# Optimization experiments

Hardware: AMD Instinct MI355X
Metric: run time of the kernel (lower is better)

The kernel has to match this reference:

```python
import jax, jax.numpy as jnp
import numpy as np

B, L = 8, 512
EMB, NHEAD, HD = 512, 8, 64
FFN, NL = 2048, 6
VOCAB, NRE, RING_START, PAD, MAXLEN = 45, 20, 24, 0, 512
NOUT0 = VOCAB - NRE  # 25
NEG = -jnp.inf


def _ln(x, g, b, eps=1e-5):
    m = jnp.mean(x, -1, keepdims=True)
    v = jnp.mean((x - m) ** 2, -1, keepdims=True)
    return (x - m) * jax.lax.rsqrt(v + eps) * g + b


def setup_inputs():
    key = jax.random.key(0)
    ks = jax.random.split(key, 24)
    p = lambda k, shape: jax.random.normal(k, shape, jnp.float32) * 0.02
    return {
        "sequences": jax.random.randint(ks[0], (B, L), 1, VOCAB),  # avoid PAD=0
        "count_sequences": jax.random.randint(ks[1], (B, L), 0, MAXLEN),
        "graph_mask_sequences": jax.random.bernoulli(ks[2], 0.05, (B, L, VOCAB)),
        "valence_mask_sequences": jax.random.bernoulli(ks[3], 0.05, (B, L, VOCAB)),
        "linear_loc_squares": jax.random.randint(ks[4], (B, L, L), 0, MAXLEN + 1),
        "up_loc_squares": jax.random.randint(ks[5], (B, L, L), 0, MAXLEN + 1),
        "down_loc_squares": jax.random.randint(ks[6], (B, L, L), 0, MAXLEN + 1),
        "tok_emb": p(ks[7], (VOCAB, EMB)),
        "cnt_emb": p(ks[8], (MAXLEN, EMB)),
        "lin_loc_emb": p(ks[9], (MAXLEN + 1, NHEAD)),
        "up_loc_emb": p(ks[10], (MAXLEN + 1, NHEAD)),
        "down_loc_emb": p(ks[11], (MAXLEN + 1, NHEAD)),
        "in_proj_w": p(ks[12], (NL, 3 * EMB, EMB)),
        "in_proj_b": jnp.zeros((NL, 3 * EMB), jnp.float32),
        "out_w": p(ks[13], (NL, EMB, EMB)),
        "out_b": jnp.zeros((NL, EMB), jnp.float32),
        "ln1_g": jnp.ones((NL, EMB), jnp.float32),
        "ln1_b": jnp.zeros((NL, EMB), jnp.float32),
        "ln2_g": jnp.ones((NL, EMB), jnp.float32),
        "ln2_b": jnp.zeros((NL, EMB), jnp.float32),
        "ffn_w1": p(ks[14], (NL, FFN, EMB)),
        "ffn_b1": jnp.zeros((NL, FFN), jnp.float32),
        "ffn_w2": p(ks[15], (NL, EMB, FFN)),
        "ffn_b2": jnp.zeros((NL, EMB), jnp.float32),
        "fin_g": jnp.ones((EMB,), jnp.float32),
        "fin_b": jnp.zeros((EMB,), jnp.float32),
        "gen_w": p(ks[16], (NOUT0, EMB)),
        "gen_b": jnp.zeros((NOUT0,), jnp.float32),
        "ring_w0": p(ks[17], (EMB, EMB)),
        "ring_b0": jnp.zeros((EMB,), jnp.float32),
        "ring_w1": p(ks[18], (EMB, EMB)),
        "ring_b1": jnp.zeros((EMB,), jnp.float32),
    }


def _forward(tok_emb, cnt_emb, lin_loc_emb, up_loc_emb, down_loc_emb,
             in_proj_w, in_proj_b, out_w, out_b, ln1_g, ln1_b, ln2_g, ln2_b,
             ffn_w1, ffn_b1, ffn_w2, ffn_b2, fin_g, fin_b, gen_w, gen_b,
             ring_w0, ring_b0, ring_w1, ring_b1,
             sequences, count_sequences, graph_mask_sequences,
             valence_mask_sequences, linear_loc_squares, up_loc_squares,
             down_loc_squares):
    scale_e = jnp.sqrt(jnp.float32(EMB))
    x = tok_emb[sequences] * scale_e + cnt_emb[count_sequences] * scale_e  # (B,L,E)

    # per-head additive attention bias from three (B,L,L) index lookups
    bias = lin_loc_emb[linear_loc_squares] + up_loc_emb[up_loc_squares] + down_loc_emb[down_loc_squares]  # (B,L,L,H)
    bias = jnp.transpose(bias, (0, 3, 1, 2))  # (B,H,Lq,Lk)
    causal = jnp.tril(jnp.ones((L, L), bool))
    attn_bias = jnp.where(causal[None, None], bias, NEG)
    pad = sequences == PAD  # key padding
    attn_bias = jnp.where(pad[:, None, None, :], NEG, attn_bias)

    inv_sqrt_hd = 1.0 / jnp.sqrt(jnp.float32(HD))
    for i in range(NL):  # post-norm TransformerEncoderLayer, gelu
        qkv = jnp.einsum('ble,fe->blf', x, in_proj_w[i]) + in_proj_b[i]
        q, k, v = jnp.split(qkv, 3, axis=-1)
        q = q.reshape(B, L, NHEAD, HD)
        k = k.reshape(B, L, NHEAD, HD)
        v = v.reshape(B, L, NHEAD, HD)
        scores = jnp.einsum('bqhd,bkhd->bhqk', q, k) * inv_sqrt_hd + attn_bias
        a = jax.nn.softmax(scores, axis=-1)
        ctx = jnp.einsum('bhqk,bkhd->bqhd', a, v).reshape(B, L, EMB)
        attn_out = jnp.einsum('ble,fe->blf', ctx, out_w[i]) + out_b[i]
        x = _ln(x + attn_out, ln1_g[i], ln1_b[i])
        h = jax.nn.gelu(jnp.einsum('ble,fe->blf', x, ffn_w1[i]) + ffn_b1[i], approximate=False)
        ff = jnp.einsum('blf,ef->ble', h, ffn_w2[i]) + ffn_b2[i]
        x = _ln(x + ff, ln2_g[i], ln2_b[i])
    x = _ln(x, fin_g, fin_b)

    logits0 = jnp.einsum('ble,oe->blo', x, gen_w) + gen_b  # (B,L,NOUT0)

    # EdgeLogitLayer: scatter ring-start projections into NRE slots
    out0 = jnp.einsum('ble,he->blh', x, ring_w0) + ring_b0
    out1_ = jnp.einsum('ble,he->blh', x, ring_w1) + ring_b1
    ring_start = sequences == RING_START
    idx = jnp.where(ring_start, jnp.cumsum(ring_start.astype(jnp.int32), axis=1), 0)  # (B,L)
    bidx = jnp.arange(B)[:, None]
    slots = jnp.zeros((B, NRE + 1, EMB), x.dtype).at[bidx, idx].set(out1_, mode='drop')
    ring_tab = slots[:, 1:]  # drop slot 0 (non-ring-start writes)
    logits1 = jnp.einsum('ble,bre->blr', out0, ring_tab) * (EMB ** -0.5)

    logits = jnp.concatenate([logits0, logits1], axis=2)  # (B,L,VOCAB)
    logits = jnp.where(graph_mask_sequences, NEG, logits)
    logits = jnp.where(valence_mask_sequences, NEG, logits)
    return logits


def reference(sequences, count_sequences, graph_mask_sequences, valence_mask_sequences,
              linear_loc_squares, up_loc_squares, down_loc_squares,
              tok_emb, cnt_emb, lin_loc_emb, up_loc_emb, down_loc_emb,
              in_proj_w, in_proj_b, out_w, out_b, ln1_g, ln1_b, ln2_g, ln2_b,
              ffn_w1, ffn_b1, ffn_w2, ffn_b2, fin_g, fin_b, gen_w, gen_b,
              ring_w0, ring_b0, ring_w1, ring_b1):
    return _forward(tok_emb, cnt_emb, lin_loc_emb, up_loc_emb, down_loc_emb,
                    in_proj_w, in_proj_b, out_w, out_b, ln1_g, ln1_b, ln2_g, ln2_b,
                    ffn_w1, ffn_b1, ffn_w2, ffn_b2, fin_g, fin_b, gen_w, gen_b,
                    ring_w0, ring_b0, ring_w1, ring_b1,
                    sequences, count_sequences, graph_mask_sequences,
                    valence_mask_sequences, linear_loc_squares, up_loc_squares,
                    down_loc_squares)
```

## Files before the change

### kernel.cpp

```cpp
#include <hip/hip_runtime.h>
#include <cmath>

#define BB 8
#define LL 512
#define EMB 512
#define NHEAD 8
#define HD 64
#define FFN 2048
#define NL 6
#define VOCAB 45
#define NRE 20
#define RING_START 24
#define NOUT0 25
#define BL 4096

#define BIG_NEG -1.0e30f

typedef __bf16 bf16x8 __attribute__((ext_vector_type(8)));
typedef __bf16 bf16x4 __attribute__((ext_vector_type(4)));
typedef float f32x4 __attribute__((ext_vector_type(4)));

__device__ __forceinline__ void ld_g2l(const __bf16* g, __bf16* l) {
  __builtin_amdgcn_global_load_lds(
      (const __attribute__((address_space(1))) unsigned int*)g,
      (__attribute__((address_space(3))) unsigned int*)l, 16, 0, 0);
}

__global__ __launch_bounds__(256) void megacast_kernel(
    const float* __restrict__ s0, const float* __restrict__ s1,
    const float* __restrict__ s2, const float* __restrict__ s3,
    const float* __restrict__ s4, const float* __restrict__ s5,
    const float* __restrict__ s6, const float* __restrict__ s7,
    const float* __restrict__ s8, __bf16* __restrict__ dw,
    __bf16* __restrict__ dt) {
  const int gid = blockIdx.x * 256 + threadIdx.x;
  const int szs[9] = {589824, 196608, 786432, 786432, 32768,
                      32768,  513,    513,    513};
  const float* srcs[9] = {s0, s1, s2, s3, s4, s5, s6, s7, s8};
  int seg = 0, base = 0;
  while (seg < 9 && gid >= base + szs[seg]) { base += szs[seg]; seg++; }
  if (seg >= 9) return;
  const int local = gid - base;
  const float* src = srcs[seg];
  const float4 a = ((const float4*)src)[local * 2];
  const float4 b = ((const float4*)src)[local * 2 + 1];
  bf16x8 v;
  v[0] = (__bf16)a.x; v[1] = (__bf16)a.y; v[2] = (__bf16)a.z; v[3] = (__bf16)a.w;
  v[4] = (__bf16)b.x; v[5] = (__bf16)b.y; v[6] = (__bf16)b.z; v[7] = (__bf16)b.w;
  __bf16* dst = (seg < 6) ? (dw + (size_t)base * 8 + (size_t)local * 8)
                          : (dt + (size_t)(seg - 6) * 4104 + (size_t)local * 8);
  *(bf16x8*)dst = v;
}

__global__ __launch_bounds__(128) void embed_kernel(
    const int* __restrict__ seq, const int* __restrict__ cnt,
    const float* __restrict__ tok_emb, const float* __restrict__ cnt_emb,
    float* __restrict__ x, __bf16* __restrict__ xb) {
  const int row = blockIdx.x;
  const int t = seq[row];
  const int c = cnt[row];
  const float scale = 22.627416997969522f;
  const int j = threadIdx.x * 4;
  float4 tv = *(const float4*)(tok_emb + (size_t)t * EMB + j);
  float4 cv = *(const float4*)(cnt_emb + (size_t)c * EMB + j);
  float4 o;
  o.x = (tv.x + cv.x) * scale;
  o.y = (tv.y + cv.y) * scale;
  o.z = (tv.z + cv.z) * scale;
  o.w = (tv.w + cv.w) * scale;
  *(float4*)(x + (size_t)row * EMB + j) = o;
  bf16x4 h;
  h[0] = (__bf16)o.x; h[1] = (__bf16)o.y; h[2] = (__bf16)o.z; h[3] = (__bf16)o.w;
  *(bf16x4*)(xb + (size_t)row * EMB + j) = h;
}

__global__ __launch_bounds__(256) void bias_kernel(
    const int* __restrict__ lin_sq, const int* __restrict__ up_sq,
    const int* __restrict__ down_sq,
    const __bf16* __restrict__ tl16, const __bf16* __restrict__ tu16,
    const __bf16* __restrict__ td16,
    const int* __restrict__ seq, __bf16* __restrict__ bias) {
  __shared__ __bf16 Tl[513 * 8], Tu[513 * 8], Td[513 * 8];
  __shared__ int seqs[LL];
  const int tid = threadIdx.x;
  const int b = blockIdx.x >> 6;
  const int q0 = (blockIdx.x & 63) * 8;
  for (int i = tid; i < 513; i += 256) {
    *(bf16x8*)&Tl[i * 8] = *(const bf16x8*)&tl16[i * 8];
    *(bf16x8*)&Tu[i * 8] = *(const bf16x8*)&tu16[i * 8];
    *(bf16x8*)&Td[i * 8] = *(const bf16x8*)&td16[i * 8];
  }
  for (int i = tid; i < LL; i += 256) seqs[i] = seq[b * LL + i];
  __syncthreads();
  for (int q = q0; q < q0 + 8; q++) {
    const size_t rbase = ((size_t)(b * LL + q)) * LL;
    for (int k = tid; k <= q; k += 256) {
      const int li = lin_sq[rbase + k], ui = up_sq[rbase + k],
                di = down_sq[rbase + k];
      const bool valid = (seqs[k] != 0);
      bf16x8 a = *(const bf16x8*)&Tl[li * 8];
      bf16x8 u = *(const bf16x8*)&Tu[ui * 8];
      bf16x8 d = *(const bf16x8*)&Td[di * 8];
#pragma unroll
      for (int h = 0; h < NHEAD; h++) {
        float v = valid ? ((float)a[h] + (float)u[h] + (float)d[h])
                        : -INFINITY;
        bias[(((size_t)(b * NHEAD + h) * LL) + q) * LL + k] = (__bf16)v;
      }
    }
  }
}

template <int BM, int BN, int ACT, int OUTBF, int RES, int SPLITK, int B2>
__global__ __launch_bounds__(256) void gemm_mfma_kernel(
    const __bf16* __restrict__ A, const __bf16* __restrict__ W,
    const float* __restrict__ bias, const float* __restrict__ bias2,
    float* __restrict__ C, __bf16* __restrict__ Cb,
    const float* __restrict__ Res, int N, int K, int lda) {
  constexpr int MI = BM / 32;
  constexpr int NI = BN / 32;
  __shared__ __bf16 As[BM * 32];
  __shared__ __bf16 Ws[BN * 32];
  const int tid = threadIdx.x;
  const int lane = tid & 63, wave = tid >> 6;
  const int wm = wave >> 1, wn = wave & 1;
  const int q = lane >> 4, l15 = lane & 15;
  const int m0 = blockIdx.y * BM, n0 = blockIdx.x * BN;
  const int kz = SPLITK ? blockIdx.z : 0;

  const __bf16* Ag =
      A + (size_t)(m0 + (tid >> 2)) * lda + (tid & 3) * 8 + (size_t)kz * K;
  const __bf16* Wg =
      W + (size_t)(n0 + (tid >> 2)) * lda + (tid & 3) * 8 + (size_t)kz * K;
  __bf16* Al = &As[tid * 8];
  __bf16* Wl = &Ws[tid * 8];

  f32x4 acc[MI][NI] = {};

  for (int k0 = 0; k0 < K; k0 += 32) {
    ld_g2l(Ag + k0, Al);
    if (BM == 128) ld_g2l(Ag + k0 + (size_t)64 * lda, Al + 2048);
    ld_g2l(Wg + k0, Wl);
    if (BN == 128) ld_g2l(Wg + k0 + (size_t)64 * lda, Wl + 2048);
    __syncthreads();
    bf16x8 af[MI], bfr[NI];
#pragma unroll
    for (int mi = 0; mi < MI; mi++)
      af[mi] =
          *(const bf16x8*)&As[(wm * (BM / 2) + mi * 16 + l15) * 32 + q * 8];
#pragma unroll
    for (int ni = 0; ni < NI; ni++)
      bfr[ni] =
          *(const bf16x8*)&Ws[(wn * (BN / 2) + ni * 16 + l15) * 32 + q * 8];
#pragma unroll
    for (int mi = 0; mi < MI; mi++)
#pragma unroll
      for (int ni = 0; ni < NI; ni++)
        acc[mi][ni] = __builtin_amdgcn_mfma_f32_16x16x32_bf16(
            af[mi], bfr[ni], acc[mi][ni], 0, 0, 0);
    __syncthreads();
  }

  float* Cz = SPLITK ? (C + (size_t)kz * ((size_t)BL * N)) : C;
#pragma unroll
  for (int ni = 0; ni < NI; ni++) {
    const int n = n0 + wn * (BN / 2) + ni * 16 + l15;
    float bv = 0.f;
    if (!SPLITK || kz == 0)
      bv = (B2 && n >= EMB) ? bias2[n - EMB] : bias[n];
#pragma unroll
    for (int mi = 0; mi < MI; mi++) {
#pragma unroll
      for (int r = 0; r < 4; r++) {
        const int m = m0 + wm * (BM / 2) + mi * 16 + q * 4 + r;
        float v = acc[mi][ni][r] + bv;
        if (RES && (!SPLITK || kz == 0)) v += Res[(size_t)m * N + n];
        if (ACT == 1) v = 0.5f * v * (1.0f + erff(v * 0.70710678118654752f));
        if (OUTBF)
          Cb[(size_t)m * N + n] = (__bf16)v;
        else
          Cz[(size_t)m * N + n] = v;
      }
    }
  }
}

__global__ __launch_bounds__(256) void attn_tile_kernel(
    const __bf16* __restrict__ qkv, const __bf16* __restrict__ bias,
    __bf16* __restrict__ Po, float2* __restrict__ Pml) {
  __shared__ __bf16 Qs[64][72];
  __shared__ __bf16 Ks[64][72];
  __shared__ __bf16 Vt[64][72];
  __shared__ __bf16 Ps[64][72];
  const int tid = threadIdx.x;
  const int lane = tid & 63, w = tid >> 6;
  const int q = lane >> 4, l15 = lane & 15;
  const int bh = blockIdx.y;
  const int b = bh >> 3, h = bh & 7;
  const int pidx = blockIdx.x;
  int qt = 0, acc0 = 0;
  while (acc0 + qt + 1 <= pidx) { acc0 += qt + 1; qt++; }
  const int kt = pidx - acc0;
  const int q0 = qt * 64, k0 = kt * 64;
  const bool diag = (qt == kt);
  const int slot = (bh * 8 + qt) * 8 + kt;
  const float inv_sqrt_hd = 0.125f;

  {
    const int row = tid >> 2, c0 = (tid & 3) * 16;
    const __bf16* qsrc = qkv + (size_t)(b * LL + q0 + row) * 1536 + h * HD + c0;
    *(bf16x8*)&Qs[row][c0] = *(const bf16x8*)qsrc;
    *(bf16x8*)&Qs[row][c0 + 8] = *(const bf16x8*)(qsrc + 8);
    const __bf16* src = qkv + (size_t)(b * LL + k0 + row) * 1536 + h * HD;
    bf16x8 kv0 = *(const bf16x8*)(src + 512 + c0);
    bf16x8 kv1 = *(const bf16x8*)(src + 512 + c0 + 8);
    bf16x8 vv0 = *(const bf16x8*)(src + 1024 + c0);
    bf16x8 vv1 = *(const bf16x8*)(src + 1024 + c0 + 8);
    *(bf16x8*)&Ks[row][c0] = kv0;
    *(bf16x8*)&Ks[row][c0 + 8] = kv1;
#pragma unroll
    for (int j = 0; j < 8; j++) {
      Vt[c0 + j][row] = vv0[j];
      Vt[c0 + 8 + j][row] = vv1[j];
    }
  }
  __syncthreads();

  f32x4 s4[4] = {};
  {
    bf16x8 aq0 = *(const bf16x8*)&Qs[w * 16 + l15][q * 8];
    bf16x8 aq1 = *(const bf16x8*)&Qs[w * 16 + l15][32 + q * 8];
#pragma unroll
    for (int ni = 0; ni < 4; ni++) {
      bf16x8 bk0 = *(const bf16x8*)&Ks[ni * 16 + l15][q * 8];
      bf16x8 bk1 = *(const bf16x8*)&Ks[ni * 16 + l15][32 + q * 8];
      s4[ni] = __builtin_amdgcn_mfma_f32_16x16x32_bf16(aq0, bk0, s4[ni], 0, 0, 0);
      s4[ni] = __builtin_amdgcn_mfma_f32_16x16x32_bf16(aq1, bk1, s4[ni], 0, 0, 0);
    }
  }

  const size_t bbase = ((size_t)bh * LL + (q0 + w * 16 + q * 4)) * LL + k0;
#pragma unroll
  for (int r = 0; r < 4; r++) {
    const int qrow = w * 16 + q * 4 + r;
    float sv[4];
#pragma unroll
    for (int ni = 0; ni < 4; ni++) {
      sv[ni] = s4[ni][r] * inv_sqrt_hd +
               (float)bias[bbase + (size_t)r * LL + ni * 16 + l15];
      if (diag && (ni * 16 + l15 > qrow)) sv[ni] = -INFINITY;
    }
    float tm = fmaxf(fmaxf(sv[0], sv[1]), fmaxf(sv[2], sv[3]));
#pragma unroll
    for (int off = 1; off < 16; off <<= 1)
      tm = fmaxf(tm, __shfl_xor(tm, off, 16));
    float rs = 0.f;
#pragma unroll
    for (int ni = 0; ni < 4; ni++) {
      const float p = expf(sv[ni] - tm);
      Ps[qrow][ni * 16 + l15] = (__bf16)p;
      rs += p;
    }
#pragma unroll
    for (int off = 1; off < 16; off <<= 1) rs += __shfl_xor(rs, off, 16);
    if (l15 == 0)
      Pml[(size_t)slot * 64 + qrow] = make_float2(tm, rs);
  }
  __syncthreads();

  f32x4 o4[4] = {};
  {
    bf16x8 ap0 = *(const bf16x8*)&Ps[w * 16 + l15][q * 8];
    bf16x8 ap1 = *(const bf16x8*)&Ps[w * 16 + l15][32 + q * 8];
#pragma unroll
    for (int ni = 0; ni < 4; ni++) {
      bf16x8 bv0 = *(const bf16x8*)&Vt[ni * 16 + l15][q * 8];
      bf16x8 bv1 = *(const bf16x8*)&Vt[ni * 16 + l15][32 + q * 8];
      o4[ni] = __builtin_amdgcn_mfma_f32_16x16x32_bf16(ap0, bv0, o4[ni], 0, 0, 0);
      o4[ni] = __builtin_amdgcn_mfma_f32_16x16x32_bf16(ap1, bv1, o4[ni], 0, 0, 0);
    }
  }
#pragma unroll
  for (int r = 0; r < 4; r++) {
    __bf16* dst = Po + (size_t)slot * 4096 + (w * 16 + q * 4 + r) * 64 + l15;
#pragma unroll
    for (int ni = 0; ni < 4; ni++) dst[ni * 16] = (__bf16)o4[ni][r];
  }
}

__global__ __launch_bounds__(256) void attn_combine_kernel(
    const __bf16* __restrict__ Po, const float2* __restrict__ Pml,
    __bf16* __restrict__ ctx) {
  const int tid = threadIdx.x;
  const int bh = blockIdx.x >> 3;
  const int qt = blockIdx.x & 7;
  const int b = bh >> 3, h = bh & 7;
  const int nkt = qt + 1;
  const int slot0 = (bh * 8 + qt) * 8;
  __shared__ float wls[8][64];
  __shared__ float invl[64];
  if (tid < 64) {
    float m = -3.0e38f;
    for (int kt = 0; kt < nkt; kt++)
      m = fmaxf(m, Pml[(size_t)(slot0 + kt) * 64 + tid].x);
    float l = 0.f;
    for (int kt = 0; kt < nkt; kt++) {
      const float2 ml = Pml[(size_t)(slot0 + kt) * 64 + tid];
      const float wk = expf(ml.x - m);
      wls[kt][tid] = wk;
      l += ml.y * wk;
    }
    invl[tid] = 1.0f / l;
  }
  __syncthreads();
  const int row = tid >> 2, d0 = (tid & 3) * 16;
  float acc[16] = {};
  for (int kt = 0; kt < nkt; kt++) {
    const __bf16* src = Po + (size_t)(slot0 + kt) * 4096 + row * 64 + d0;
    const float wk = wls[kt][row];
    bf16x8 v0 = *(const bf16x8*)src;
    bf16x8 v1 = *(const bf16x8*)(src + 8);
#pragma unroll
    for (int j = 0; j < 8; j++) {
      acc[j] += (float)v0[j] * wk;
      acc[8 + j] += (float)v1[j] * wk;
    }
  }
  const float il = invl[row];
  bf16x8 o0, o1;
#pragma unroll
  for (int j = 0; j < 8; j++) {
    o0[j] = (__bf16)(acc[j] * il);
    o1[j] = (__bf16)(acc[8 + j] * il);
  }
  __bf16* dst = ctx + (size_t)(b * LL + qt * 64 + row) * EMB + h * HD + d0;
  *(bf16x8*)dst = o0;
  *(bf16x8*)(dst + 8) = o1;
}

template <int NSUM>
__global__ __launch_bounds__(256) void add_ln_kernel(
    const float* __restrict__ xin, const float* __restrict__ g,
    const float* __restrict__ bta, float* __restrict__ out,
    __bf16* __restrict__ outb) {
  const int row = blockIdx.x;
  const int tid = threadIdx.x;
  float v0 = 0.f, v1 = 0.f;
#pragma unroll
  for (int sId = 0; sId < NSUM; sId++) {
    const float* xr = xin + (size_t)sId * BL * EMB + (size_t)row * EMB;
    v0 += xr[tid * 2];
    v1 += xr[tid * 2 + 1];
  }
  float s = v0 + v1, ss = v0 * v0 + v1 * v1;
#pragma unroll
  for (int off = 1; off < 64; off <<= 1) {
    s += __shfl_xor(s, off, 64);
    ss += __shfl_xor(ss, off, 64);
  }
  __shared__ float sbuf[8];
  const int wave = tid >> 6, lane = tid & 63;
  if (lane == 0) { sbuf[wave] = s; sbuf[4 + wave] = ss; }
  __syncthreads();
  s = sbuf[0] + sbuf[1] + sbuf[2] + sbuf[3];
  ss = sbuf[4] + sbuf[5] + sbuf[6] + sbuf[7];
  const float mean = s * (1.0f / EMB);
  const float var = ss * (1.0f / EMB) - mean * mean;
  const float rstd = rsqrtf(var + 1e-5f);
  const float o0 = (v0 - mean) * rstd * g[tid * 2] + bta[tid * 2];
  const float o1 = (v1 - mean) * rstd * g[tid * 2 + 1] + bta[tid * 2 + 1];
  float* orow = out + (size_t)row * EMB;
  orow[tid * 2] = o0;
  orow[tid * 2 + 1] = o1;
  if (outb) {
    __bf16* brow = outb + (size_t)row * EMB;
    brow[tid * 2] = (__bf16)o0;
    brow[tid * 2 + 1] = (__bf16)o1;
  }
}

__global__ __launch_bounds__(256) void ring_scatter_kernel(
    const int* __restrict__ seq, const float* __restrict__ o01,
    float* __restrict__ ring_tab) {
  const int b = blockIdx.x;
  const int tid = threadIdx.x;
  float* rt = ring_tab + (size_t)b * NRE * EMB;
  for (int i = tid; i < NRE * EMB; i += 256) rt[i] = 0.f;
  __shared__ int pos[NRE];
  __shared__ int cntr;
  if (tid == 0) {
    int c = 0;
    for (int l = 0; l < LL; l++) {
      if (seq[b * LL + l] == RING_START) {
        c++;
        if (c <= NRE) pos[c - 1] = l;
      }
    }
    cntr = (c < NRE) ? c : NRE;
  }
  __syncthreads();
  const int n = cntr;
  for (int r = 0; r < n; r++) {
    const float* src = o01 + (size_t)(b * LL + pos[r]) * 1024 + 512;
    for (int i = tid; i < EMB; i += 256) rt[r * EMB + i] = src[i];
  }
}

__global__ __launch_bounds__(256) void head_kernel(
    const float* __restrict__ xf, const float* __restrict__ o01,
    const float* __restrict__ ring_tab, const float* __restrict__ gen_w,
    const float* __restrict__ gen_b, const int* __restrict__ gmask,
    const int* __restrict__ vmask, float* __restrict__ out) {
  const int row = blockIdx.x;
  const int b = row >> 9;
  const int tid = threadIdx.x;
  __shared__ float xr[EMB], o0s[EMB];
  {
    float2 a = ((const float2*)(xf + (size_t)row * EMB))[tid];
    ((float2*)xr)[tid] = a;
    float2 c = ((const float2*)(o01 + (size_t)row * 1024))[tid];
    ((float2*)o0s)[tid] = c;
  }
  __syncthreads();
  const int wave = tid >> 6, lane = tid & 63;
  for (int o = wave; o < VOCAB; o += 4) {
    const float* wrow;
    const float* src;
    float bv, scale;
    if (o < NOUT0) {
      wrow = gen_w + (size_t)o * EMB;
      bv = gen_b[o];
      src = xr;
      scale = 1.0f;
    } else {
      wrow = ring_tab + ((size_t)b * NRE + (o - NOUT0)) * EMB;
      bv = 0.0f;
      src = o0s;
      scale = 0.044194173824159216f;
    }
    float sum = 0.f;
#pragma unroll
    for (int j = 0; j < 8; j++) {
      const int d = lane + 64 * j;
      sum += src[d] * wrow[d];
    }
#pragma unroll
    for (int off = 1; off < 64; off <<= 1) sum += __shfl_xor(sum, off, 64);
    if (lane == 0) {
      float v = sum * scale + bv;
      const size_t oidx = (size_t)row * VOCAB + o;
      if (gmask[oidx] != 0 || vmask[oidx] != 0) v = BIG_NEG;
      out[oidx] = v;
    }
  }
}

extern "C" void kernel_launch(void* const* d_in, const int* in_sizes, int n_in,
                              void* d_out, int out_size, void* d_ws,
                              size_t ws_size, hipStream_t stream) {
  const int* seq = (const int*)d_in[0];
  const int* cnt = (const int*)d_in[1];
  const int* gmask = (const int*)d_in[2];
  const int* vmask = (const int*)d_in[3];
  const int* lin_sq = (const int*)d_in[4];
  const int* up_sq = (const int*)d_in[5];
  const int* down_sq = (const int*)d_in[6];
  const float* tok_emb = (const float*)d_in[7];
  const float* cnt_emb = (const float*)d_in[8];
  const float* lin_e = (const float*)d_in[9];
  const float* up_e = (const float*)d_in[10];
  const float* down_e = (const float*)d_in[11];
  const float* in_proj_w = (const float*)d_in[12];
  const float* in_proj_b = (const float*)d_in[13];
  const float* out_w = (const float*)d_in[14];
  const float* out_b = (const float*)d_in[15];
  const float* ln1_g = (const float*)d_in[16];
  const float* ln1_b = (const float*)d_in[17];
  const float* ln2_g = (const float*)d_in[18];
  const float* ln2_b = (const float*)d_in[19];
  const float* ffn_w1 = (const float*)d_in[20];
  const float* ffn_b1 = (const float*)d_in[21];
  const float* ffn_w2 = (const float*)d_in[22];
  const float* ffn_b2 = (const float*)d_in[23];
  const float* fin_g = (const float*)d_in[24];
  const float* fin_b = (const float*)d_in[25];
  const float* gen_w = (const float*)d_in[26];
  const float* gen_b = (const float*)d_in[27];
  const float* ring_w0 = (const float*)d_in[28];
  const float* ring_b0 = (const float*)d_in[29];
  const float* ring_w1 = (const float*)d_in[30];
  const float* ring_b1 = (const float*)d_in[31];

  char* p = (char*)d_ws;
  auto alloc_f = [&](size_t n) { float* r = (float*)p; p += n * 4; return r; };
  auto alloc_h = [&](size_t n) { __bf16* r = (__bf16*)p; p += n * 2; return r; };

  float* x = alloc_f((size_t)BL * EMB);
  float* pbuf = alloc_f((size_t)2 * BL * EMB);
  float* xfb = alloc_f((size_t)BL * EMB);
  float* o01b = alloc_f((size_t)BL * 1024);
  float* ringb = alloc_f((size_t)BB * NRE * EMB);
  float2* attn_pml = (float2*)alloc_f((size_t)4096 * 64 * 2);
  __bf16* attn_po = alloc_h((size_t)4096 * 4096);
  __bf16* biasb = alloc_h((size_t)BB * NHEAD * LL * LL);
  __bf16* xb = alloc_h((size_t)BL * EMB);
  __bf16* qkvb16 = alloc_h((size_t)BL * 3 * EMB);
  __bf16* ctxb = alloc_h((size_t)BL * EMB);
  __bf16* hb = alloc_h((size_t)BL * FFN);
  __bf16* xfb16 = alloc_h((size_t)BL * EMB);
  __bf16* wqkv = alloc_h((size_t)NL * 3 * EMB * EMB);
  __bf16* wout = alloc_h((size_t)NL * EMB * EMB);
  __bf16* wf1 = alloc_h((size_t)NL * FFN * EMB);
  __bf16* wf2 = alloc_h((size_t)NL * EMB * FFN);
  __bf16* wr01 = alloc_h((size_t)2 * EMB * EMB);
  __bf16* tl16 = hb;
  __bf16* tu16 = hb + 4104;
  __bf16* td16 = hb + 8208;

  megacast_kernel<<<9478, 256, 0, stream>>>(
      in_proj_w, out_w, ffn_w1, ffn_w2, ring_w0, ring_w1, lin_e, up_e, down_e,
      wqkv, tl16);

  embed_kernel<<<BL, 128, 0, stream>>>(seq, cnt, tok_emb, cnt_emb, x, xb);
  bias_kernel<<<BB * 64, 256, 0, stream>>>(lin_sq, up_sq, down_sq, tl16, tu16,
                                           td16, seq, biasb);

  for (int i = 0; i < NL; i++) {
    gemm_mfma_kernel<64, 128, 0, 1, 0, 0, 0><<<dim3(12, 64), 256, 0, stream>>>(
        xb, wqkv + (size_t)i * 3 * EMB * EMB, in_proj_b + (size_t)i * 3 * EMB,
        nullptr, nullptr, qkvb16, nullptr, 3 * EMB, EMB, EMB);
    attn_tile_kernel<<<dim3(36, 64), 256, 0, stream>>>(qkvb16, biasb, attn_po,
                                                       attn_pml);
    attn_combine_kernel<<<512, 256, 0, stream>>>(attn_po, attn_pml, ctxb);
    gemm_mfma_kernel<64, 64, 0, 0, 1, 1, 0><<<dim3(8, 64, 2), 256, 0, stream>>>(
        ctxb, wout + (size_t)i * EMB * EMB, out_b + (size_t)i * EMB, nullptr,
        pbuf, nullptr, x, EMB, EMB / 2, EMB);
    add_ln_kernel<2><<<BL, 256, 0, stream>>>(
        pbuf, ln1_g + (size_t)i * EMB, ln1_b + (size_t)i * EMB, x, xb);
    gemm_mfma_kernel<64, 128, 1, 1, 0, 0, 0><<<dim3(16, 64), 256, 0, stream>>>(
        xb, wf1 + (size_t)i * FFN * EMB, ffn_b1 + (size_t)i * FFN, nullptr,
        nullptr, hb, nullptr, FFN, EMB, EMB);
    gemm_mfma_kernel<64, 64, 0, 0, 1, 1, 0><<<dim3(8, 64, 2), 256, 0, stream>>>(
        hb, wf2 + (size_t)i * EMB * FFN, ffn_b2 + (size_t)i * EMB, nullptr,
        pbuf, nullptr, x, EMB, FFN / 2, FFN);
    add_ln_kernel<2><<<BL, 256, 0, stream>>>(
        pbuf, ln2_g + (size_t)i * EMB, ln2_b + (size_t)i * EMB, x, xb);
  }

  add_ln_kernel<1><<<BL, 256, 0, stream>>>(x, fin_g, fin_b, xfb, xfb16);
  gemm_mfma_kernel<64, 128, 0, 0, 0, 0, 1><<<dim3(8, 64), 256, 0, stream>>>(
      xfb16, wr01, ring_b0, ring_b1, o01b, nullptr, nullptr, 1024, EMB, EMB);
  ring_scatter_kernel<<<BB, 256, 0, stream>>>(seq, o01b, ringb);
  head_kernel<<<BL, 256, 0, stream>>>(xfb, o01b, ringb, gen_w, gen_b, gmask,
                                      vmask, (float*)d_out);
}
```

Baseline: 1.028 ms.

## Fuse attention into single online-softmax kernel and drop split-K in projections

Replaces the per-tile attention kernel and its separate combine kernel with one flash-style kernel that loops over key tiles with an online softmax and writes the normalized context directly. This removes the partial-output and max/sum round trips through global memory and one launch per layer. Query tiles are ordered so the longest causal rows are scheduled first. The out-projection and FFN2 GEMMs also drop split-K, halving their grids, so their add+LN kernels now read one partial buffer; this trades fewer launches' worth of traffic for less parallelism and a serial per-block key loop.

```diff
diff --git a/kernel.cpp b/kernel.cpp
--- a/kernel.cpp
+++ b/kernel.cpp
@@ -185,157 +185,126 @@
   }
 }
 
-__global__ __launch_bounds__(256) void attn_tile_kernel(
+__global__ __launch_bounds__(256) void attn_fused_kernel(
     const __bf16* __restrict__ qkv, const __bf16* __restrict__ bias,
-    __bf16* __restrict__ Po, float2* __restrict__ Pml) {
-  __shared__ __bf16 Qs[64][72];
+    __bf16* __restrict__ ctx) {
   __shared__ __bf16 Ks[64][72];
   __shared__ __bf16 Vt[64][72];
   __shared__ __bf16 Ps[64][72];
   const int tid = threadIdx.x;
   const int lane = tid & 63, w = tid >> 6;
   const int q = lane >> 4, l15 = lane & 15;
-  const int bh = blockIdx.y;
+  int id = blockIdx.x;
+  int bh, qt;
+  if (id < 256) { bh = id >> 2; qt = 7 - (id & 3); }
+  else { id -= 256; bh = id >> 2; qt = id & 3; }
   const int b = bh >> 3, h = bh & 7;
-  const int pidx = blockIdx.x;
-  int qt = 0, acc0 = 0;
-  while (acc0 + qt + 1 <= pidx) { acc0 += qt + 1; qt++; }
-  const int kt = pidx - acc0;
-  const int q0 = qt * 64, k0 = kt * 64;
-  const bool diag = (qt == kt);
-  const int slot = (bh * 8 + qt) * 8 + kt;
+  const int q0 = qt * 64;
   const float inv_sqrt_hd = 0.125f;
 
+  const int srow = tid >> 2, c0 = (tid & 3) * 16;
   {
-    const int row = tid >> 2, c0 = (tid & 3) * 16;
-    const __bf16* qsrc = qkv + (size_t)(b * LL + q0 + row) * 1536 + h * HD + c0;
-    *(bf16x8*)&Qs[row][c0] = *(const bf16x8*)qsrc;
-    *(bf16x8*)&Qs[row][c0 + 8] = *(const bf16x8*)(qsrc + 8);
-    const __bf16* src = qkv + (size_t)(b * LL + k0 + row) * 1536 + h * HD;
-    bf16x8 kv0 = *(const bf16x8*)(src + 512 + c0);
-    bf16x8 kv1 = *(const bf16x8*)(src + 512 + c0 + 8);
-    bf16x8 vv0 = *(const bf16x8*)(src + 1024 + c0);
-    bf16x8 vv1 = *(const bf16x8*)(src + 1024 + c0 + 8);
-    *(bf16x8*)&Ks[row][c0] = kv0;
-    *(bf16x8*)&Ks[row][c0 + 8] = kv1;
-#pragma unroll
-    for (int j = 0; j < 8; j++) {
-      Vt[c0 + j][row] = vv0[j];
-      Vt[c0 + 8 + j][row] = vv1[j];
-    }
+    const __bf16* qsrc =
+        qkv + (size_t)(b * LL + q0 + srow) * 1536 + h * HD + c0;
+    *(bf16x8*)&Ps[srow][c0] = *(const bf16x8*)qsrc;
+    *(bf16x8*)&Ps[srow][c0 + 8] = *(const bf16x8*)(qsrc + 8);
   }
   __syncthreads();
-
-  f32x4 s4[4] = {};
-  {
-    bf16x8 aq0 = *(const bf16x8*)&Qs[w * 16 + l15][q * 8];
-    bf16x8 aq1 = *(const bf16x8*)&Qs[w * 16 + l15][32 + q * 8];
+  const bf16x8 aq0 = *(const bf16x8*)&Ps[w * 16 + l15][q * 8];
+  const bf16x8 aq1 = *(const bf16x8*)&Ps[w * 16 + l15][32 + q * 8];
+
+  f32x4 o4[4] = {};
+  float m[4], l[4];
+#pragma unroll
+  for (int r = 0; r < 4; r++) { m[r] = -INFINITY; l[r] = 0.f; }
+
+  for (int kt = 0; kt <= qt; kt++) {
+    const int k0 = kt * 64;
+    __syncthreads();
+    {
+      const __bf16* src = qkv + (size_t)(b * LL + k0 + srow) * 1536 + h * HD;
+      bf16x8 kv0 = *(const bf16x8*)(src + 512 + c0);
+      bf16x8 kv1 = *(const bf16x8*)(src + 512 + c0 + 8);
+      bf16x8 vv0 = *(const bf16x8*)(src + 1024 + c0);
+      bf16x8 vv1 = *(const bf16x8*)(src + 1024 + c0 + 8);
+      *(bf16x8*)&Ks[srow][c0] = kv0;
+      *(bf16x8*)&Ks[srow][c0 + 8] = kv1;
+#pragma unroll
+      for (int j = 0; j < 8; j++) {
+        Vt[c0 + j][srow] = vv0[j];
+        Vt[c0 + 8 + j][srow] = vv1[j];
+      }
+    }
+    __syncthreads();
+
+    f32x4 s4[4] = {};
 #pragma unroll
     for (int ni = 0; ni < 4; ni++) {
       bf16x8 bk0 = *(const bf16x8*)&Ks[ni * 16 + l15][q * 8];
       bf16x8 bk1 = *(const bf16x8*)&Ks[ni * 16 + l15][32 + q * 8];
-      s4[ni] = __builtin_amdgcn_mfma_f32_16x16x32_bf16(aq0, bk0, s4[ni], 0, 0, 0);
-      s4[ni] = __builtin_amdgcn_mfma_f32_16x16x32_bf16(aq1, bk1, s4[ni], 0, 0, 0);
-    }
-  }
-
-  const size_t bbase = ((size_t)bh * LL + (q0 + w * 16 + q * 4)) * LL + k0;
+      s4[ni] =
+          __builtin_amdgcn_mfma_f32_16x16x32_bf16(aq0, bk0, s4[ni], 0, 0, 0);
+      s4[ni] =
+          __builtin_amdgcn_mfma_f32_16x16x32_bf16(aq1, bk1, s4[ni], 0, 0, 0);
+    }
+
+    const bool diag = (kt == qt);
+    const size_t bbase = ((size_t)bh * LL + (q0 + w * 16 + q * 4)) * LL + k0;
+#pragma unroll
+    for (int r = 0; r < 4; r++) {
+      const int qrow = w * 16 + q * 4 + r;
+      float sv[4];
+#pragma unroll
+      for (int ni = 0; ni < 4; ni++) {
+        sv[ni] = s4[ni][r] * inv_sqrt_hd +
+                 (float)bias[bbase + (size_t)r * LL + ni * 16 + l15];
+        if (diag && (ni * 16 + l15 > qrow)) sv[ni] = -INFINITY;
+      }
+      float tm = fmaxf(fmaxf(sv[0], sv[1]), fmaxf(sv[2], sv[3]));
+#pragma unroll
+      for (int off = 1; off < 16; off <<= 1)
+        tm = fmaxf(tm, __shfl_xor(tm, off, 16));
+      const float mnew = fmaxf(m[r], tm);
+      const float alpha = expf(m[r] - mnew);
+      float rs = 0.f;
+#pragma unroll
+      for (int ni = 0; ni < 4; ni++) {
+        const float p = expf(sv[ni] - mnew);
+        Ps[qrow][ni * 16 + l15] = (__bf16)p;
+        rs += p;
+      }
+#pragma unroll
+      for (int off = 1; off < 16; off <<= 1) rs += __shfl_xor(rs, off, 16);
+      l[r] = l[r] * alpha + rs;
+      m[r] = mnew;
+#pragma unroll
+      for (int ni = 0; ni < 4; ni++) o4[ni][r] *= alpha;
+    }
+    __syncthreads();
+
+    {
+      bf16x8 ap0 = *(const bf16x8*)&Ps[w * 16 + l15][q * 8];
+      bf16x8 ap1 = *(const bf16x8*)&Ps[w * 16 + l15][32 + q * 8];
+#pragma unroll
+      for (int ni = 0; ni < 4; ni++) {
+        bf16x8 bv0 = *(const bf16x8*)&Vt[ni * 16 + l15][q * 8];
+        bf16x8 bv1 = *(const bf16x8*)&Vt[ni * 16 + l15][32 + q * 8];
+        o4[ni] =
+            __builtin_amdgcn_mfma_f32_16x16x32_bf16(ap0, bv0, o4[ni], 0, 0, 0);
+        o4[ni] =
+            __builtin_amdgcn_mfma_f32_16x16x32_bf16(ap1, bv1, o4[ni], 0, 0, 0);
+      }
+    }
+  }
+
 #pragma unroll
   for (int r = 0; r < 4; r++) {
     const int qrow = w * 16 + q * 4 + r;
-    float sv[4];
-#pragma unroll
-    for (int ni = 0; ni < 4; ni++) {
-      sv[ni] = s4[ni][r] * inv_sqrt_hd +
-               (float)bias[bbase + (size_t)r * LL + ni * 16 + l15];
-      if (diag && (ni * 16 + l15 > qrow)) sv[ni] = -INFINITY;
-    }
-    float tm = fmaxf(fmaxf(sv[0], sv[1]), fmaxf(sv[2], sv[3]));
-#pragma unroll
-    for (int off = 1; off < 16; off <<= 1)
-      tm = fmaxf(tm, __shfl_xor(tm, off, 16));
-    float rs = 0.f;
-#pragma unroll
-    for (int ni = 0; ni < 4; ni++) {
-      const float p = expf(sv[ni] - tm);
-      Ps[qrow][ni * 16 + l15] = (__bf16)p;
-      rs += p;
-    }
-#pragma unroll
-    for (int off = 1; off < 16; off <<= 1) rs += __shfl_xor(rs, off, 16);
-    if (l15 == 0)
-      Pml[(size_t)slot * 64 + qrow] = make_float2(tm, rs);
-  }
-  __syncthreads();
-
-  f32x4 o4[4] = {};
-  {
-    bf16x8 ap0 = *(const bf16x8*)&Ps[w * 16 + l15][q * 8];
-    bf16x8 ap1 = *(const bf16x8*)&Ps[w * 16 + l15][32 + q * 8];
-#pragma unroll
-    for (int ni = 0; ni < 4; ni++) {
-      bf16x8 bv0 = *(const bf16x8*)&Vt[ni * 16 + l15][q * 8];
-      bf16x8 bv1 = *(const bf16x8*)&Vt[ni * 16 + l15][32 + q * 8];
-      o4[ni] = __builtin_amdgcn_mfma_f32_16x16x32_bf16(ap0, bv0, o4[ni], 0, 0, 0);
-      o4[ni] = __builtin_amdgcn_mfma_f32_16x16x32_bf16(ap1, bv1, o4[ni], 0, 0, 0);
-    }
-  }
-#pragma unroll
-  for (int r = 0; r < 4; r++) {
-    __bf16* dst = Po + (size_t)slot * 4096 + (w * 16 + q * 4 + r) * 64 + l15;
-#pragma unroll
-    for (int ni = 0; ni < 4; ni++) dst[ni * 16] = (__bf16)o4[ni][r];
-  }
-}
-
-__global__ __launch_bounds__(256) void attn_combine_kernel(
-    const __bf16* __restrict__ Po, const float2* __restrict__ Pml,
-    __bf16* __restrict__ ctx) {
-  const int tid = threadIdx.x;
-  const int bh = blockIdx.x >> 3;
-  const int qt = blockIdx.x & 7;
-  const int b = bh >> 3, h = bh & 7;
-  const int nkt = qt + 1;
-  const int slot0 = (bh * 8 + qt) * 8;
-  __shared__ float wls[8][64];
-  __shared__ float invl[64];
-  if (tid < 64) {
-    float m = -3.0e38f;
-    for (int kt = 0; kt < nkt; kt++)
-      m = fmaxf(m, Pml[(size_t)(slot0 + kt) * 64 + tid].x);
-    float l = 0.f;
-    for (int kt = 0; kt < nkt; kt++) {
-      const float2 ml = Pml[(size_t)(slot0 + kt) * 64 + tid];
-      const float wk = expf(ml.x - m);
-      wls[kt][tid] = wk;
-      l += ml.y * wk;
-    }
-    invl[tid] = 1.0f / l;
-  }
-  __syncthreads();
-  const int row = tid >> 2, d0 = (tid & 3) * 16;
-  float acc[16] = {};
-  for (int kt = 0; kt < nkt; kt++) {
-    const __bf16* src = Po + (size_t)(slot0 + kt) * 4096 + row * 64 + d0;
-    const float wk = wls[kt][row];
-    bf16x8 v0 = *(const bf16x8*)src;
-    bf16x8 v1 = *(const bf16x8*)(src + 8);
-#pragma unroll
-    for (int j = 0; j < 8; j++) {
-      acc[j] += (float)v0[j] * wk;
-      acc[8 + j] += (float)v1[j] * wk;
-    }
-  }
-  const float il = invl[row];
-  bf16x8 o0, o1;
-#pragma unroll
-  for (int j = 0; j < 8; j++) {
-    o0[j] = (__bf16)(acc[j] * il);
-    o1[j] = (__bf16)(acc[8 + j] * il);
-  }
-  __bf16* dst = ctx + (size_t)(b * LL + qt * 64 + row) * EMB + h * HD + d0;
-  *(bf16x8*)dst = o0;
-  *(bf16x8*)(dst + 8) = o1;
+    const float inv = 1.0f / l[r];
+    __bf16* dst = ctx + (size_t)(b * LL + q0 + qrow) * EMB + h * HD + l15;
+#pragma unroll
+    for (int ni = 0; ni < 4; ni++) dst[ni * 16] = (__bf16)(o4[ni][r] * inv);
+  }
 }
 
 template <int NSUM>
@@ -496,12 +465,10 @@
   auto alloc_h = [&](size_t n) { __bf16* r = (__bf16*)p; p += n * 2; return r; };
 
   float* x = alloc_f((size_t)BL * EMB);
-  float* pbuf = alloc_f((size_t)2 * BL * EMB);
+  float* pbuf = alloc_f((size_t)BL * EMB);
   float* xfb = alloc_f((size_t)BL * EMB);
   float* o01b = alloc_f((size_t)BL * 1024);
   float* ringb = alloc_f((size_t)BB * NRE * EMB);
-  float2* attn_pml = (float2*)alloc_f((size_t)4096 * 64 * 2);
-  __bf16* attn_po = alloc_h((size_t)4096 * 4096);
   __bf16* biasb = alloc_h((size_t)BB * NHEAD * LL * LL);
   __bf16* xb = alloc_h((size_t)BL * EMB);
   __bf16* qkvb16 = alloc_h((size_t)BL * 3 * EMB);
@@ -529,21 +496,19 @@
     gemm_mfma_kernel<64, 128, 0, 1, 0, 0, 0><<<dim3(12, 64), 256, 0, stream>>>(
         xb, wqkv + (size_t)i * 3 * EMB * EMB, in_proj_b + (size_t)i * 3 * EMB,
         nullptr, nullptr, qkvb16, nullptr, 3 * EMB, EMB, EMB);
-    attn_tile_kernel<<<dim3(36, 64), 256, 0, stream>>>(qkvb16, biasb, attn_po,
-                                                       attn_pml);
-    attn_combine_kernel<<<512, 256, 0, stream>>>(attn_po, attn_pml, ctxb);
-    gemm_mfma_kernel<64, 64, 0, 0, 1, 1, 0><<<dim3(8, 64, 2), 256, 0, stream>>>(
+    attn_fused_kernel<<<512, 256, 0, stream>>>(qkvb16, biasb, ctxb);
+    gemm_mfma_kernel<64, 64, 0, 0, 1, 0, 0><<<dim3(8, 64), 256, 0, stream>>>(
         ctxb, wout + (size_t)i * EMB * EMB, out_b + (size_t)i * EMB, nullptr,
-        pbuf, nullptr, x, EMB, EMB / 2, EMB);
-    add_ln_kernel<2><<<BL, 256, 0, stream>>>(
+        pbuf, nullptr, x, EMB, EMB, EMB);
+    add_ln_kernel<1><<<BL, 256, 0, stream>>>(
         pbuf, ln1_g + (size_t)i * EMB, ln1_b + (size_t)i * EMB, x, xb);
     gemm_mfma_kernel<64, 128, 1, 1, 0, 0, 0><<<dim3(16, 64), 256, 0, stream>>>(
         xb, wf1 + (size_t)i * FFN * EMB, ffn_b1 + (size_t)i * FFN, nullptr,
         nullptr, hb, nullptr, FFN, EMB, EMB);
-    gemm_mfma_kernel<64, 64, 0, 0, 1, 1, 0><<<dim3(8, 64, 2), 256, 0, stream>>>(
+    gemm_mfma_kernel<64, 64, 0, 0, 1, 0, 0><<<dim3(8, 64), 256, 0, stream>>>(
         hb, wf2 + (size_t)i * EMB * FFN, ffn_b2 + (size_t)i * EMB, nullptr,
-        pbuf, nullptr, x, EMB, FFN / 2, FFN);
-    add_ln_kernel<2><<<BL, 256, 0, stream>>>(
+        pbuf, nullptr, x, EMB, FFN, FFN);
+    add_ln_kernel<1><<<BL, 256, 0, stream>>>(
         pbuf, ln2_g + (size_t)i * EMB, ln2_b + (size_t)i * EMB, x, xb);
   }
 
```

New measurement: 1.073 ms. +4.3%, slower.
